# Kernel optimization log

Hardware: AMD Instinct MI355X
Metric: run time of the kernel (lower is better)

## Reference

```python
import jax, jax.numpy as jnp
import numpy as np

B, T, D = 4, 4096, 4096
G, C, K, M = 1, 4, 128, 32          # num_groups, n_splits, dw_hidden_dim, heads_per_group
I2 = 4                               # qkw inner dim = 2 * dynamic_hidden_dim (dyn_hidden = 32//16 = 2)
EPS = 1.1920929e-07                  # torch F.rms_norm default eps for fp32


def _rms_norm(x):
    # F.rms_norm over last dim, no learned scale
    return x * jax.lax.rsqrt(jnp.mean(x * x, axis=-1, keepdims=True) + EPS)


def setup_inputs() -> dict:
    key = jax.random.key(0)
    k0, k1, k2, k3 = jax.random.split(key, 4)
    dw1_std = np.sqrt(2.0 / (D + K))
    qkw_std = 0.02 / (np.sqrt(2 * 32 * 2) * (32 + 2))
    dd_std = 0.05 * np.sqrt(2.0 / (32 + D))
    return {
        "query_vec": jax.random.normal(k0, (B, T, D), dtype=jnp.float32),
        "dw1": jax.random.normal(k1, (D, G, C, K), dtype=jnp.float32) * dw1_std,
        "qkw": jax.random.normal(k2, (G, C, K, I2, M), dtype=jnp.float32) * qkw_std,
        "dd": jax.random.normal(k3, (D, G, M * C), dtype=jnp.float32) * dd_std,
        "norm_scale": jnp.ones((G,), dtype=jnp.float32) * 0.001,
    }


def reference(query_vec, dw1, qkw, dd, norm_scale):
    # dw_hidden: [B,T,G,C,K]
    dw_hidden = jnp.einsum('btd,dgck->btgck', query_vec, dw1)
    dw_hidden = jax.nn.gelu(dw_hidden, approximate=False)  # torch nn.GELU() is exact
    # w: [B,T,G,C,I2,M]
    w = jnp.einsum('btgck,gckim->btgcim', dw_hidden, qkw)
    half = qkw.shape[-2] // 2
    w1 = _rms_norm(w[..., :half, :])
    w2 = _rms_norm(w[..., half:, :]) * norm_scale  # norm_scale [G]=(1,) broadcasts over M
    # squeeze group dim (keep_group_dim=False) -> [B,T,C,I,M]
    w1 = w1[:, :, 0]
    w2 = w2[:, :, 0]
    # unbind along C: order pre_q, pre_k, post_q, post_k; key-wise pieces are discarded
    pre_qw1, post_qw1 = w1[:, :, 0], w1[:, :, 2]
    pre_qw2, post_qw2 = w2[:, :, 0], w2[:, :, 2]
    # dd: [B,T,G,M*C] -> tanh -> squeeze G -> split 4
    dd_out = jnp.tanh(jnp.einsum('btd,dgm->btgm', query_vec, dd))[:, :, 0]
    pre_qdd = dd_out[..., 0 * M:1 * M]
    post_qdd = dd_out[..., 2 * M:3 * M]
    # pack all live outputs into one array [B, T, 2*(2*I*M) + 2*M]
    flat = lambda a: a.reshape(a.shape[0], a.shape[1], -1)
    return jnp.concatenate(
        [flat(pre_qw1), flat(pre_qw2), pre_qdd,
         flat(post_qw1), flat(post_qw2), post_qdd], axis=-1)
```

## Files before the change

### kernel.cpp

```cpp
#include <hip/hip_runtime.h>
#include <cstdint>
#include <cstddef>

typedef __bf16 bf16x8 __attribute__((ext_vector_type(8)));
typedef float f32x4 __attribute__((ext_vector_type(4)));

#define D_DIM 4096
#define NCOL 320
#define BM 32
#define NKT 128
#define EPS_F 1.1920929e-07f
#define HS 136
#define STG 24576
#define RING 3
#define SMEM (RING * STG)

__device__ __forceinline__ void gld16(const void* g, void* l) {
  __builtin_amdgcn_global_load_lds(
      (const __attribute__((address_space(1))) unsigned int*)g,
      (__attribute__((address_space(3))) unsigned int*)l,
      16, 0, 0);
}

__global__ void dwp_pack(const float* __restrict__ dw1,
                         const float* __restrict__ qkw,
                         const float* __restrict__ dd,
                         __bf16* __restrict__ Wp,
                         __bf16* __restrict__ Qt) {
  const int b = blockIdx.x;
  const int t = threadIdx.x;
  if (b < 128) {
    __shared__ __bf16 tile[10240];
    const int kt = b;
    const int kk = t >> 3;
    const int d = kt * 32 + kk;
    const int u = kk >> 3;
#pragma unroll
    for (int j = 0; j < 5; ++j) {
      const int n0 = ((t & 7) + j * 8) * 8;
      const float* src;
      if (n0 < 128)      src = dw1 + (size_t)d * 512 + n0;
      else if (n0 < 256) src = dw1 + (size_t)d * 512 + 128 + n0;
      else if (n0 < 288) src = dd + (size_t)d * 128 + (n0 - 256);
      else               src = dd + (size_t)d * 128 + (n0 - 224);
      f32x4 v0 = *(const f32x4*)src;
      f32x4 v1 = *(const f32x4*)(src + 4);
#pragma unroll
      for (int q = 0; q < 8; ++q) {
        const int n = n0 + q;
        const int pos = n * 32 + ((u ^ ((n >> 1) & 3)) << 3) + (kk & 7);
        tile[pos] = (__bf16)((q < 4) ? v0[q] : v1[q - 4]);
      }
    }
    __syncthreads();
    __bf16* dst = Wp + (size_t)kt * 10240;
#pragma unroll
    for (int k = 0; k < 5; ++k) {
      const int u16 = t + k * 256;
      *(bf16x8*)(dst + u16 * 8) = *(const bf16x8*)(tile + u16 * 8);
    }
  } else {
#pragma unroll
    for (int ii = 0; ii < 16; ++ii) {
      const int q = t + ii * 256;
      const int c2 = q >> 11;
      const int rem = q & 2047;
      const int n = rem >> 4;
      const int k0 = (rem & 15) * 8;
      const float* src = qkw + (size_t)c2 * 32768 + (size_t)k0 * 128 + n;
      bf16x8 v;
#pragma unroll
      for (int j = 0; j < 8; ++j) v[j] = (__bf16)src[(size_t)j * 128];
      *(bf16x8*)(Qt + (size_t)c2 * 16384 + (size_t)n * 128 + k0) = v;
    }
  }
}

__global__ __launch_bounds__(512, 4) void dwp_main(
    const float* __restrict__ X,
    const __bf16* __restrict__ Wp,
    const __bf16* __restrict__ Qt,
    const float* __restrict__ NS,
    float* __restrict__ Out) {
  extern __shared__ __align__(16) unsigned char lds[];
  const int t = threadIdx.x;
  const int w = t >> 6;
  const int l = t & 63;
  const int lq = l >> 4;
  const int lm = l & 15;
  const int m0 = blockIdx.x * BM;

  const int rg = w >> 2;
  const int cg = w & 3;
  const int cbase = cg * 80;

  const char* gsrc[3];
  int gstep[3];
  unsigned ldsoff[3];
#pragma unroll
  for (int i = 0; i < 3; ++i) {
    const int c = w * 3 + i;
    if (c < 4) {
      const int row = c * 8 + (l >> 3);
      const int u = (l & 7) ^ (row & 7);
      gsrc[i] = (const char*)(X + (size_t)(m0 + row) * D_DIM) + u * 16;
      gstep[i] = 128;
      ldsoff[i] = (unsigned)(c * 1024);
    } else {
      const int cb = c - 4;
      gsrc[i] = (const char*)Wp + cb * 1024 + (size_t)l * 16;
      gstep[i] = 20480;
      ldsoff[i] = (unsigned)(4096 + cb * 1024);
    }
  }

  unsigned aoff0, aoff1, boff[5];
  {
    const int row = rg * 16 + lm;
    aoff0 = (unsigned)(row * 128 + (((lq * 2 + 0) ^ (lm & 7)) * 16));
    aoff1 = (unsigned)(row * 128 + (((lq * 2 + 1) ^ (lm & 7)) * 16));
  }
#pragma unroll
  for (int ct = 0; ct < 5; ++ct) {
    const int n = cbase + ct * 16 + lm;
    boff[ct] = (unsigned)(4096 + n * 64 + ((lq ^ ((n >> 1) & 3)) << 4));
  }

  f32x4 acc[5];
#pragma unroll
  for (int ct = 0; ct < 5; ++ct) acc[ct] = (f32x4){0.f, 0.f, 0.f, 0.f};

  auto issue = [&](int kt, int slot) {
    unsigned char* base = lds + slot * STG;
#pragma unroll
    for (int i = 0; i < 3; ++i)
      gld16(gsrc[i] + (size_t)kt * gstep[i], base + ldsoff[i]);
  };

  auto body = [&](int kt, int slot) {
    const unsigned char* cb = lds + slot * STG;
    bf16x8 a, b[5];
    f32x4 x0 = *(const f32x4*)(cb + aoff0);
    f32x4 x1 = *(const f32x4*)(cb + aoff1);
#pragma unroll
    for (int j = 0; j < 4; ++j) {
      a[j] = (__bf16)x0[j];
      a[4 + j] = (__bf16)x1[j];
    }
#pragma unroll
    for (int ct = 0; ct < 5; ++ct) b[ct] = *(const bf16x8*)(cb + boff[ct]);
#pragma unroll
    for (int ct = 0; ct < 5; ++ct)
      acc[ct] =
          __builtin_amdgcn_mfma_f32_16x16x32_bf16(a, b[ct], acc[ct], 0, 0, 0);
  };

  issue(0, 0);
  issue(1, 1);

  int rb = 0;
  for (int kt = 0; kt < NKT - 1; ++kt) {
    asm volatile("s_waitcnt vmcnt(3)" ::: "memory");
    asm volatile("s_barrier" ::: "memory");
    if (kt + 2 < NKT) {
      int ri = rb + 2; if (ri >= RING) ri -= RING;
      issue(kt + 2, ri);
    }
    body(kt, rb);
    ++rb; if (rb == RING) rb = 0;
  }
  asm volatile("s_waitcnt vmcnt(0)" ::: "memory");
  asm volatile("s_barrier" ::: "memory");
  body(NKT - 1, rb);

  __syncthreads();

  const float ns = NS[0];

#pragma unroll
  for (int ct = 0; ct < 5; ++ct) {
    const int ncol = cbase + ct * 16 + lm;
    const int rowb = rg * 16 + lq * 4;
    f32x4 v = acc[ct];
    if (ncol < 256) {
      const int c2 = ncol >> 7;
      const int kcol = ncol & 127;
#pragma unroll
      for (int j = 0; j < 4; ++j) {
        float x = v[j];
        float g = 0.5f * x * (1.0f + erff(x * 0.70710678118f));
        *(__bf16*)(lds + (size_t)((c2 * 32 + rowb + j) * HS + kcol) * 2) = (__bf16)g;
      }
    } else {
      const int nd = ncol - 256;
      const int off = (nd < 32) ? (128 + nd) : (256 + nd);
#pragma unroll
      for (int j = 0; j < 4; ++j)
        Out[(size_t)(m0 + rowb + j) * NCOL + off] = tanhf(v[j]);
    }
  }
  __syncthreads();

  const int c2b = w >> 2;
  const int iq = w & 3;
  const int nnb = iq * 32;
  f32x4 acc2[2][2];
#pragma unroll
  for (int rt = 0; rt < 2; ++rt)
#pragma unroll
    for (int ct = 0; ct < 2; ++ct) acc2[rt][ct] = (f32x4){0.f, 0.f, 0.f, 0.f};

#pragma unroll
  for (int ks = 0; ks < 4; ++ks) {
    bf16x8 a2[2], b2[2];
#pragma unroll
    for (int rt = 0; rt < 2; ++rt)
      a2[rt] = *(const bf16x8*)(lds +
               (size_t)((c2b * 32 + rt * 16 + lm) * HS + ks * 32 + lq * 8) * 2);
#pragma unroll
    for (int ct = 0; ct < 2; ++ct)
      b2[ct] = *(const bf16x8*)(Qt + (size_t)c2b * 16384 +
               (size_t)(nnb + ct * 16 + lm) * 128 + ks * 32 + lq * 8);
#pragma unroll
    for (int rt = 0; rt < 2; ++rt)
#pragma unroll
      for (int ct = 0; ct < 2; ++ct)
        acc2[rt][ct] =
            __builtin_amdgcn_mfma_f32_16x16x32_bf16(a2[rt], b2[ct], acc2[rt][ct], 0, 0, 0);
  }

  const float sce = (iq >= 2) ? ns : 1.0f;
#pragma unroll
  for (int rt = 0; rt < 2; ++rt) {
    f32x4 va = acc2[rt][0];
    f32x4 vb = acc2[rt][1];
#pragma unroll
    for (int j = 0; j < 4; ++j) {
      float s = va[j] * va[j] + vb[j] * vb[j];
      s += __shfl_xor(s, 1);
      s += __shfl_xor(s, 2);
      s += __shfl_xor(s, 4);
      s += __shfl_xor(s, 8);
      const float sc = rsqrtf(s * (1.0f / 32.0f) + EPS_F) * sce;
      const size_t row = (size_t)(m0 + rt * 16 + lq * 4 + j);
      const int off = c2b * 160 + iq * 32;
      Out[row * NCOL + off + lm] = va[j] * sc;
      Out[row * NCOL + off + 16 + lm] = vb[j] * sc;
    }
  }
}

extern "C" void kernel_launch(void* const* d_in, const int* in_sizes, int n_in,
                              void* d_out, int out_size, void* d_ws, size_t ws_size,
                              hipStream_t stream) {
  const float* qv  = (const float*)d_in[0];
  const float* dw1 = (const float*)d_in[1];
  const float* qkw = (const float*)d_in[2];
  const float* dd  = (const float*)d_in[3];
  const float* ns  = (const float*)d_in[4];
  float* out = (float*)d_out;

  __bf16* Wp = (__bf16*)d_ws;
  __bf16* Qt = Wp + (size_t)4096 * 320;

  hipFuncSetAttribute((const void*)dwp_main,
                      hipFuncAttributeMaxDynamicSharedMemorySize, SMEM);

  dwp_pack<<<129, 256, 0, stream>>>(dw1, qkw, dd, Wp, Qt);
  dwp_main<<<512, 512, SMEM, stream>>>(qv, Wp, Qt, ns, out);
}
```

Baseline: 443.8 us.

## Double row tile to 64 with 1024-thread blocks and deeper 4-slot ring

Doubles the rows per block from 32 to 64, so each weight tile loaded into LDS is reused by twice as many rows and total weight traffic through L2 halves. Blocks grow to 16 waves over 256 blocks, the load work is redistributed across waves, and the prefetch ring grows from 3 to 4 stages (prefetch distance 3) with per-wave vmcnt waits. The epilogue GELU staging and second-stage MFMA are remapped to the 64-row tile. The trade-off is fewer blocks (256 on a large GPU), larger LDS per block (about 112KB) and lower occupancy, which may hurt latency hiding.

```diff
diff --git a/kernel.cpp b/kernel.cpp
--- a/kernel.cpp
+++ b/kernel.cpp
@@ -7,12 +7,13 @@
 
 #define D_DIM 4096
 #define NCOL 320
-#define BM 32
+#define BM 64
 #define NKT 128
 #define EPS_F 1.1920929e-07f
 #define HS 136
-#define STG 24576
-#define RING 3
+#define ABYTES 8192
+#define STG 28672
+#define RING 4
 #define SMEM (RING * STG)
 
 __device__ __forceinline__ void gld16(const void* g, void* l) {
@@ -76,7 +77,7 @@
   }
 }
 
-__global__ __launch_bounds__(512, 4) void dwp_main(
+__global__ __launch_bounds__(1024, 4) void dwp_main(
     const float* __restrict__ X,
     const __bf16* __restrict__ Wp,
     const __bf16* __restrict__ Qt,
@@ -94,23 +95,26 @@
   const int cg = w & 3;
   const int cbase = cg * 80;
 
-  const char* gsrc[3];
-  int gstep[3];
-  unsigned ldsoff[3];
-#pragma unroll
-  for (int i = 0; i < 3; ++i) {
-    const int c = w * 3 + i;
-    if (c < 4) {
+  const int cnt = (w < 12) ? 2 : 1;
+  const char* gsrc[2];
+  int gstep[2];
+  unsigned ldsoff[2];
+#pragma unroll
+  for (int i = 0; i < 2; ++i) {
+    const int c = w + i * 16;
+    if (i < cnt && c < 8) {
       const int row = c * 8 + (l >> 3);
       const int u = (l & 7) ^ (row & 7);
       gsrc[i] = (const char*)(X + (size_t)(m0 + row) * D_DIM) + u * 16;
       gstep[i] = 128;
       ldsoff[i] = (unsigned)(c * 1024);
-    } else {
-      const int cb = c - 4;
+    } else if (i < cnt) {
+      const int cb = c - 8;
       gsrc[i] = (const char*)Wp + cb * 1024 + (size_t)l * 16;
       gstep[i] = 20480;
-      ldsoff[i] = (unsigned)(4096 + cb * 1024);
+      ldsoff[i] = (unsigned)(ABYTES + cb * 1024);
+    } else {
+      gsrc[i] = nullptr; gstep[i] = 0; ldsoff[i] = 0;
     }
   }
 
@@ -123,7 +127,7 @@
 #pragma unroll
   for (int ct = 0; ct < 5; ++ct) {
     const int n = cbase + ct * 16 + lm;
-    boff[ct] = (unsigned)(4096 + n * 64 + ((lq ^ ((n >> 1) & 3)) << 4));
+    boff[ct] = (unsigned)(ABYTES + n * 64 + ((lq ^ ((n >> 1) & 3)) << 4));
   }
 
   f32x4 acc[5];
@@ -133,8 +137,9 @@
   auto issue = [&](int kt, int slot) {
     unsigned char* base = lds + slot * STG;
 #pragma unroll
-    for (int i = 0; i < 3; ++i)
-      gld16(gsrc[i] + (size_t)kt * gstep[i], base + ldsoff[i]);
+    for (int i = 0; i < 2; ++i)
+      if (i < cnt)
+        gld16(gsrc[i] + (size_t)kt * gstep[i], base + ldsoff[i]);
   };
 
   auto body = [&](int kt, int slot) {
@@ -157,21 +162,26 @@
 
   issue(0, 0);
   issue(1, 1);
-
-  int rb = 0;
-  for (int kt = 0; kt < NKT - 1; ++kt) {
-    asm volatile("s_waitcnt vmcnt(3)" ::: "memory");
+  issue(2, 2);
+
+  for (int kt = 0; kt < NKT - 3; ++kt) {
+    if (w < 12) asm volatile("s_waitcnt vmcnt(4)" ::: "memory");
+    else        asm volatile("s_waitcnt vmcnt(2)" ::: "memory");
     asm volatile("s_barrier" ::: "memory");
-    if (kt + 2 < NKT) {
-      int ri = rb + 2; if (ri >= RING) ri -= RING;
-      issue(kt + 2, ri);
-    }
-    body(kt, rb);
-    ++rb; if (rb == RING) rb = 0;
-  }
+    issue(kt + 3, (kt + 3) & 3);
+    body(kt, kt & 3);
+  }
+  if (w < 12) asm volatile("s_waitcnt vmcnt(4)" ::: "memory");
+  else        asm volatile("s_waitcnt vmcnt(2)" ::: "memory");
+  asm volatile("s_barrier" ::: "memory");
+  body(NKT - 3, (NKT - 3) & 3);
+  if (w < 12) asm volatile("s_waitcnt vmcnt(2)" ::: "memory");
+  else        asm volatile("s_waitcnt vmcnt(1)" ::: "memory");
+  asm volatile("s_barrier" ::: "memory");
+  body(NKT - 2, (NKT - 2) & 3);
   asm volatile("s_waitcnt vmcnt(0)" ::: "memory");
   asm volatile("s_barrier" ::: "memory");
-  body(NKT - 1, rb);
+  body(NKT - 1, (NKT - 1) & 3);
 
   __syncthreads();
 
@@ -189,7 +199,7 @@
       for (int j = 0; j < 4; ++j) {
         float x = v[j];
         float g = 0.5f * x * (1.0f + erff(x * 0.70710678118f));
-        *(__bf16*)(lds + (size_t)((c2 * 32 + rowb + j) * HS + kcol) * 2) = (__bf16)g;
+        *(__bf16*)(lds + (size_t)((c2 * 64 + rowb + j) * HS + kcol) * 2) = (__bf16)g;
       }
     } else {
       const int nd = ncol - 256;
@@ -201,8 +211,9 @@
   }
   __syncthreads();
 
-  const int c2b = w >> 2;
-  const int iq = w & 3;
+  const int c2b = w >> 3;
+  const int iq = (w >> 1) & 3;
+  const int rh = w & 1;
   const int nnb = iq * 32;
   f32x4 acc2[2][2];
 #pragma unroll
@@ -216,7 +227,7 @@
 #pragma unroll
     for (int rt = 0; rt < 2; ++rt)
       a2[rt] = *(const bf16x8*)(lds +
-               (size_t)((c2b * 32 + rt * 16 + lm) * HS + ks * 32 + lq * 8) * 2);
+               (size_t)((c2b * 64 + rh * 32 + rt * 16 + lm) * HS + ks * 32 + lq * 8) * 2);
 #pragma unroll
     for (int ct = 0; ct < 2; ++ct)
       b2[ct] = *(const bf16x8*)(Qt + (size_t)c2b * 16384 +
@@ -242,7 +253,7 @@
       s += __shfl_xor(s, 4);
       s += __shfl_xor(s, 8);
       const float sc = rsqrtf(s * (1.0f / 32.0f) + EPS_F) * sce;
-      const size_t row = (size_t)(m0 + rt * 16 + lq * 4 + j);
+      const size_t row = (size_t)(m0 + rh * 32 + rt * 16 + lq * 4 + j);
       const int off = c2b * 160 + iq * 32;
       Out[row * NCOL + off + lm] = va[j] * sc;
       Out[row * NCOL + off + 16 + lm] = vb[j] * sc;
@@ -267,5 +278,5 @@
                       hipFuncAttributeMaxDynamicSharedMemorySize, SMEM);
 
   dwp_pack<<<129, 256, 0, stream>>>(dw1, qkw, dd, Wp, Qt);
-  dwp_main<<<512, 512, SMEM, stream>>>(qv, Wp, Qt, ns, out);
-}
+  dwp_main<<<256, 1024, SMEM, stream>>>(qv, Wp, Qt, ns, out);
+}
```

Result: faster. 426.0 us (-4.0%).
